# Kernel tuning notes

Hardware: AMD Instinct MI355X
Metric: run time of the kernel (lower is better)

## Reference

```python
import jax, jax.numpy as jnp
import numpy as np

N, T, I, H = 32, 2048, 256, 512


def setup_inputs() -> dict:
    key = jax.random.key(0)
    k1, k2, k3, k4, k5 = jax.random.split(key, 5)
    x = jax.random.normal(k1, (N, T, I), dtype=jnp.float32)
    initial = jax.random.normal(k2, (N, H), dtype=jnp.float32)
    # nn.Linear default init: U(-1/sqrt(fan_in), 1/sqrt(fan_in))
    s_ih = 1.0 / np.sqrt(I)
    s_hh = 1.0 / np.sqrt(H)
    W_ih = jax.random.uniform(k3, (H, I), jnp.float32, -s_ih, s_ih)
    b_ih = jax.random.uniform(k4, (H,), jnp.float32, -s_ih, s_ih)
    W_hh = jax.random.uniform(k5, (H, H), jnp.float32, -s_hh, s_hh)
    return {"x": x, "initial": initial, "W_ih": W_ih, "b_ih": b_ih, "W_hh": W_hh}


def reference(x, initial, W_ih, b_ih, W_hh):
    # Precompute input projections for all timesteps: [N, T, H]
    proj = jnp.einsum('nti,hi->nth', x, W_ih) + b_ih
    # h_0 = initial + W_ih x_0 + b
    h0 = initial + proj[:, 0]
    # h_t = W_hh h_{t-1} + W_ih x_{t-1} + b  (note: x index is t-1, faithful to source)
    xs = jnp.swapaxes(proj[:, :-1], 0, 1)  # time-major [T-1, N, H], entries t=0..T-2

    def step(h_prev, p):
        h_new = h_prev @ W_hh.T + p
        return h_new, h_new

    _, hs = jax.lax.scan(step, h0, xs)  # [T-1, N, H]
    hiddens = jnp.concatenate([h0[:, None], jnp.swapaxes(hs, 0, 1)], axis=1)  # [N, T, H]
    return (hiddens, hiddens)
```

## Files before the change

### kernel.cpp

```cpp
#include <hip/hip_runtime.h>

#define NB 32
#define TT 2048
#define II 256
#define HH 512
#define LCH 8
#define NCH 256

typedef short s8v __attribute__((ext_vector_type(8)));
typedef short s4v __attribute__((ext_vector_type(4)));
typedef __bf16 bf8v __attribute__((ext_vector_type(8)));
typedef float f4v __attribute__((ext_vector_type(4)));

#define DEVI static __device__ __forceinline__

DEVI float bf2f(short s){ union{unsigned u; float f;} c; c.u = ((unsigned)(unsigned short)s) << 16; return c.f; }
DEVI short f2bf(float f){ union{float f; unsigned u;} c; c.f = f; unsigned u = c.u; u += 0x7FFF + ((u >> 16) & 1); return (short)(u >> 16); }
DEVI f4v fzero(){ f4v z = {0.0f,0.0f,0.0f,0.0f}; return z; }

DEVI f4v mfma16(s8v a, s8v b, f4v c){
  union{ s8v s; bf8v b; } ua, ub; ua.s = a; ub.s = b;
  return __builtin_amdgcn_mfma_f32_16x16x32_bf16(ua.b, ub.b, c, 0, 0, 0);
}

DEVI s8v packbf(f4v lo, f4v hi){
  s8v o;
  o[0]=f2bf(lo[0]); o[1]=f2bf(lo[1]); o[2]=f2bf(lo[2]); o[3]=f2bf(lo[3]);
  o[4]=f2bf(hi[0]); o[5]=f2bf(hi[1]); o[6]=f2bf(hi[2]); o[7]=f2bf(hi[3]);
  return o;
}

DEVI s8v ldfrag_bf(const short* base, int row0, int ld, int k0, int lane){
  const short* p = base + (size_t)(row0 + (lane & 15)) * ld + k0 + ((lane >> 4) << 3);
  return *(const s8v*)p;
}
DEVI s8v ldfrag_f32(const float* base, int row0, int ld, int k0, int lane){
  const float* p = base + (size_t)(row0 + (lane & 15)) * ld + k0 + ((lane >> 4) << 3);
  f4v lo = *(const f4v*)p;
  f4v hi = *(const f4v*)(p + 4);
  return packbf(lo, hi);
}
DEVI s8v ldfragX(const float* x, int t, int n0, int k0, int lane){
  const float* p = x + ((size_t)(n0 + (lane & 15))*TT + t)*II + k0 + ((lane >> 4) << 3);
  f4v lo = *(const f4v*)p;
  f4v hi = *(const f4v*)(p + 4);
  return packbf(lo, hi);
}

DEVI int swzoff(int row, int col){ return (row << 9) + ((((col >> 3) ^ (row & 7)) << 3) | (col & 7)); }

#define RAWBAR() asm volatile("s_waitcnt lgkmcnt(0)\n\ts_barrier" ::: "memory")

__global__ __launch_bounds__(256) void k_init_p1(const float* __restrict__ W,
                                                 short* __restrict__ mats, short* __restrict__ matsT){
  __shared__ short tile[64][65];
  int bx = blockIdx.x, by = blockIdx.y;
  int t = threadIdx.x;
  for(int i = 0; i < 16; ++i){
    int idx = t + 256*i;
    int rr = idx >> 6, cc = idx & 63;
    short v = f2bf(W[(size_t)(64*by + rr)*HH + 64*bx + cc]);
    tile[rr][cc] = v;
    mats[(size_t)(64*by + rr)*HH + 64*bx + cc] = v;
  }
  __syncthreads();
  for(int i = 0; i < 16; ++i){
    int idx = t + 256*i;
    int rr = idx >> 6, cc = idx & 63;
    matsT[(size_t)(64*bx + rr)*HH + 64*by + cc] = tile[cc][rr];
  }
}

__global__ __launch_bounds__(256) void k_cvt(const float* __restrict__ src, short* __restrict__ dst, int n){
  for(int i = blockIdx.x*256 + threadIdx.x; i < n; i += gridDim.x*256) dst[i] = f2bf(src[i]);
}

struct ProdArgs {
  const short* A[8]; const short* Bt[8]; short* C[8]; short* Ct[8];
};
__global__ __launch_bounds__(256) void k_prod(ProdArgs args){
  int bz = blockIdx.z;
  const short* A  = args.A[bz];
  const short* Bt = args.Bt[bz];
  short* C  = args.C[bz];
  short* Ct = args.Ct[bz];
  int wave = threadIdx.x >> 6, lane = threadIdx.x & 63;
  int mrow0 = blockIdx.x*64 + (wave & 1)*32;
  int ncol0 = blockIdx.y*128 + (wave >> 1)*64;
  f4v acc[2][4];
  for(int mi=0;mi<2;mi++) for(int j=0;j<4;j++) acc[mi][j] = fzero();
  for(int k0 = 0; k0 < HH; k0 += 32){
    s8v a0 = ldfrag_bf(A, mrow0,      HH, k0, lane);
    s8v a1 = ldfrag_bf(A, mrow0 + 16, HH, k0, lane);
    #pragma unroll
    for(int j = 0; j < 4; ++j){
      s8v b = ldfrag_bf(Bt, ncol0 + (j<<4), HH, k0, lane);
      acc[0][j] = mfma16(a0, b, acc[0][j]);
      acc[1][j] = mfma16(a1, b, acc[1][j]);
    }
  }
  int q = lane >> 4, c0 = lane & 15;
  for(int mi=0;mi<2;mi++) for(int j=0;j<4;j++) for(int r=0;r<4;r++){
    int row = mrow0 + (mi<<4) + (q<<2) + r;
    int col = ncol0 + (j<<4) + c0;
    short v = f2bf(acc[mi][j][r]);
    C [(size_t)row*HH + col] = v;
    Ct[(size_t)col*HH + row] = v;
  }
}

__global__ __launch_bounds__(512) void k_projT(const float* __restrict__ x, const short* __restrict__ Wb,
                                               const float* __restrict__ bih, const float* __restrict__ initial,
                                               short* __restrict__ projF, float* __restrict__ Y00){
  int t = blockIdx.x;
  int tid = threadIdx.x, wave = tid >> 6, lane = tid & 63;
  int q = lane >> 4, c0 = lane & 15;
  int ncol0 = wave << 6;
  f4v acc[2][4];
  #pragma unroll
  for(int mi=0;mi<2;mi++)
  #pragma unroll
  for(int j=0;j<4;j++) acc[mi][j] = fzero();
  #pragma unroll
  for(int kc = 0; kc < 8; ++kc){
    int k0 = kc << 5;
    s8v a0 = ldfragX(x, t, 0,  k0, lane);
    s8v a1 = ldfragX(x, t, 16, k0, lane);
    #pragma unroll
    for(int j = 0; j < 4; ++j){
      s8v bb = ldfrag_bf(Wb, ncol0 + (j<<4), II, k0, lane);
      acc[0][j] = mfma16(a0, bb, acc[0][j]);
      acc[1][j] = mfma16(a1, bb, acc[1][j]);
    }
  }
  float bv[4];
  #pragma unroll
  for(int j=0;j<4;++j) bv[j] = bih[ncol0 + (j<<4) + c0];
  s8v pv[4];
  #pragma unroll
  for(int mi=0;mi<2;++mi)
  #pragma unroll
  for(int j=0;j<4;++j)
  #pragma unroll
  for(int r=0;r<4;++r){
    int idx = (mi<<4) | (j<<2) | r;
    float v = acc[mi][j][r] + bv[j];
    pv[idx>>3][idx&7] = f2bf(v);
    if(t == 0){
      int n = (mi<<4) + (q<<2) + r;
      int col = ncol0 + (j<<4) + c0;
      Y00[(size_t)n*HH + col] = v + initial[(size_t)n*HH + col];
    }
  }
  short* dst = projF + (((size_t)t << 9) + tid)*32;
  #pragma unroll
  for(int g = 0; g < 4; ++g) *(s8v*)(dst + (g<<3)) = pv[g];
}

template<int PHASE, int DUAL>
__global__ __launch_bounds__(512) void k_scan(const short* __restrict__ projF,
                                              const short* __restrict__ Wb,
                                              const float* __restrict__ Zin,
                                              float* __restrict__ Yout,
                                              float* __restrict__ Yout2){
  __shared__ __align__(16) short st[NB*HH];
  __shared__ __align__(16) float fstage[PHASE==1 ? NB*HH : 4];
  int c = blockIdx.x;
  int tid = threadIdx.x, wave = tid >> 6, lane = tid & 63;
  int q = lane >> 4, c0 = lane & 15;
  int ncol0 = wave << 6;
  if constexpr(PHASE == 0){
    for(int i = tid; i < NB*HH; i += 512) st[i] = 0;
  } else {
    const float* Z = Zin + (size_t)c*NB*HH;
    #pragma unroll
    for(int rr = 0; rr < 8; ++rr){
      int fi = tid + (rr << 9);
      int rn = fi >> 7, col = (fi & 127) << 2;
      f4v v = *(const f4v*)(Z + (size_t)rn*HH + col);
      s4v sv; sv[0]=f2bf(v[0]); sv[1]=f2bf(v[1]); sv[2]=f2bf(v[2]); sv[3]=f2bf(v[3]);
      *(s4v*)(st + swzoff(rn, col)) = sv;
      if(c == 0){
        *(f4v*)(Yout + ((size_t)rn*TT)*HH + col) = v;
        if(DUAL) *(f4v*)(Yout2 + ((size_t)rn*TT)*HH + col) = v;
      }
    }
  }
  RAWBAR();
  int tmax = min(LCH, TT - 1 - LCH*c);
  for(int tl = 1; tl <= tmax; ++tl){
    int t = LCH*c + tl;
    const short* pb = projF + (((size_t)(t-1) << 9) + tid)*32;
    s8v pp[4];
    pp[0] = *(const s8v*)(pb);
    pp[1] = *(const s8v*)(pb + 8);
    pp[2] = *(const s8v*)(pb + 16);
    pp[3] = *(const s8v*)(pb + 24);
    f4v acc[2][4];
    #pragma unroll
    for(int mi=0;mi<2;mi++)
    #pragma unroll
    for(int j=0;j<4;j++) acc[mi][j] = fzero();
    #pragma unroll
    for(int kc = 0; kc < 16; ++kc){
      int k0 = kc << 5;
      int colb = k0 + (q << 3);
      s8v a0 = *(const s8v*)(st + swzoff(c0,      colb));
      s8v a1 = *(const s8v*)(st + swzoff(c0 + 16, colb));
      #pragma unroll
      for(int j = 0; j < 4; ++j){
        s8v bb = ldfrag_bf(Wb, ncol0 + (j<<4), HH, k0, lane);
        acc[0][j] = mfma16(a0, bb, acc[0][j]);
        acc[1][j] = mfma16(a1, bb, acc[1][j]);
      }
    }
    RAWBAR();
    #pragma unroll
    for(int mi=0;mi<2;++mi)
    #pragma unroll
    for(int j=0;j<4;++j)
    #pragma unroll
    for(int r=0;r<4;++r){
      int idx = (mi<<4) | (j<<2) | r;
      int rown = (mi<<4) + (q<<2) + r;
      int col  = ncol0 + (j<<4) + c0;
      float v = acc[mi][j][r] + bf2f(pp[idx>>3][idx&7]);
      st[swzoff(rown, col)] = f2bf(v);
      if constexpr(PHASE == 0){
        if(tl == LCH && c + 1 < NCH)
          Yout[((size_t)(c+1)*NB + rown)*HH + col] = v;
      } else {
        fstage[rown*HH + col] = v;
      }
    }
    if constexpr(PHASE == 1){
      RAWBAR();
      #pragma unroll
      for(int rr = 0; rr < 8; ++rr){
        int fi = tid + (rr << 9);
        int rn = fi >> 7, col = (fi & 127) << 2;
        f4v v = *(const f4v*)(fstage + (size_t)rn*HH + col);
        *(f4v*)(Yout + ((size_t)rn*TT + t)*HH + col) = v;
        if(DUAL) *(f4v*)(Yout2 + ((size_t)rn*TT + t)*HH + col) = v;
      }
    } else {
      RAWBAR();
    }
  }
}

__global__ __launch_bounds__(512) void k_ks(const float* __restrict__ Yin, float* __restrict__ Yout,
                                            const short* __restrict__ As, int s){
  __shared__ __align__(16) float fstage[NB*HH];
  int i = blockIdx.x;
  int tid = threadIdx.x;
  if(i < s){
    const float* src = Yin + (size_t)i*NB*HH;
    float* dst = Yout + (size_t)i*NB*HH;
    for(int fi = tid; fi < NB*HH/4; fi += 512)
      *(f4v*)(dst + ((size_t)fi << 2)) = *(const f4v*)(src + ((size_t)fi << 2));
    return;
  }
  int wave = tid >> 6, lane = tid & 63;
  int q = lane >> 4, c0 = lane & 15;
  int ncol0 = wave << 6;
  const float* Xp = Yin + (size_t)(i - s)*NB*HH;
  const float* Xc = Yin + (size_t)i*NB*HH;
  float* Out = Yout + (size_t)i*NB*HH;
  f4v acc[2][4];
  #pragma unroll
  for(int mi=0;mi<2;mi++)
  #pragma unroll
  for(int j=0;j<4;j++) acc[mi][j] = fzero();
  #pragma unroll
  for(int kc = 0; kc < 16; ++kc){
    int k0 = kc << 5;
    s8v a0 = ldfrag_f32(Xp, 0,  HH, k0, lane);
    s8v a1 = ldfrag_f32(Xp, 16, HH, k0, lane);
    #pragma unroll
    for(int j = 0; j < 4; ++j){
      s8v bb = ldfrag_bf(As, ncol0 + (j<<4), HH, k0, lane);
      acc[0][j] = mfma16(a0, bb, acc[0][j]);
      acc[1][j] = mfma16(a1, bb, acc[1][j]);
    }
  }
  #pragma unroll
  for(int mi=0;mi<2;++mi)
  #pragma unroll
  for(int j=0;j<4;++j)
  #pragma unroll
  for(int r=0;r<4;++r){
    int rown = (mi<<4) + (q<<2) + r;
    int col  = ncol0 + (j<<4) + c0;
    fstage[(size_t)rown*HH + col] = acc[mi][j][r];
  }
  RAWBAR();
  #pragma unroll
  for(int rr = 0; rr < 8; ++rr){
    int fi = tid + (rr << 9);
    int rn = fi >> 7, col = (fi & 127) << 2;
    f4v v = *(const f4v*)(fstage + (size_t)rn*HH + col);
    f4v xc = *(const f4v*)(Xc + (size_t)rn*HH + col);
    v = v + xc;
    *(f4v*)(Out + (size_t)rn*HH + col) = v;
  }
}

__global__ __launch_bounds__(256) void k_dup(const float* __restrict__ a, float* __restrict__ b, int n4){
  for(int i = blockIdx.x*256 + threadIdx.x; i < n4; i += gridDim.x*256)
    ((f4v*)b)[i] = ((const f4v*)a)[i];
}

extern "C" void kernel_launch(void* const* d_in, const int* in_sizes, int n_in,
                              void* d_out, int out_size, void* d_ws, size_t ws_size,
                              hipStream_t stream) {
  const float* x       = (const float*)d_in[0];
  const float* initial = (const float*)d_in[1];
  const float* Wih     = (const float*)d_in[2];
  const float* bih     = (const float*)d_in[3];
  const float* Whh     = (const float*)d_in[4];
  float* out1 = (float*)d_out;
  float* out2 = out1 + (size_t)NB*TT*HH;

  const size_t MSZ = (size_t)HH*HH;
  short* mats  = (short*)d_ws;
  short* matsT = mats + 11*MSZ;
  short* Wihb  = matsT + 11*MSZ;
  float* Y0 = (float*)(Wihb + (size_t)HH*II);
  float* Y1 = out1;
  short* projw = (short*)(Y0 + (size_t)NCH*NB*HH);
  size_t need = (size_t)((char*)(projw + (size_t)NB*TT*HH) - (char*)d_ws);
  bool dual = ws_size >= need;
  short* projF = dual ? projw : (short*)out2;

  auto M = [&](int i){ return mats  + (size_t)i*MSZ; };
  auto T = [&](int i){ return matsT + (size_t)i*MSZ; };

  k_init_p1<<<dim3(8,8), 256, 0, stream>>>(Whh, M(0), T(0));
  k_cvt<<<dim3(64), 256, 0, stream>>>(Wih, Wihb, HH*II);

  ProdArgs pa;
  for(int i = 0; i < 10; ++i){
    pa.A[0] = M(i); pa.Bt[0] = T(i); pa.C[0] = M(i+1); pa.Ct[0] = T(i+1);
    k_prod<<<dim3(8,4,1), 256, 0, stream>>>(pa);
  }

  k_projT<<<dim3(TT), 512, 0, stream>>>(x, Wihb, bih, initial, projF, Y0);
  k_scan<0,0><<<dim3(NCH), 512, 0, stream>>>(projF, M(0), nullptr, Y0, nullptr);

  float* Ya = Y0; float* Yb = Y1;
  for(int l = 0; l < 8; ++l){
    k_ks<<<dim3(NCH), 512, 0, stream>>>(Ya, Yb, M(3 + l), 1 << l);
    float* tsw = Ya; Ya = Yb; Yb = tsw;
  }

  if(dual){
    k_scan<1,1><<<dim3(NCH), 512, 0, stream>>>(projF, M(0), Y0, out1, out2);
  } else {
    k_scan<1,0><<<dim3(NCH), 512, 0, stream>>>(projF, M(0), Y0, out1, out1);
    k_dup<<<dim3(2048), 256, 0, stream>>>(out1, out2, NB*TT*HH/4);
  }
}
```

Measured before the change: 1.296 ms.

## Use nontemporal loads/stores for streaming data and drop LDS output staging in scan

Replaces ordinary global loads and stores of streamed activations, projections and outputs with nontemporal builtins across the projection, scan and Kogge-Stone kernels, to reduce cache pollution. In the phase-1 scan it also removes the fp32 LDS staging buffer and extra barrier, writing each output element straight to global memory with scalar nontemporal stores. This cuts LDS use and a barrier per timestep, but the direct scalar stores are less coalesced than the old vectorized staged writes.

Measured after the change: 1.443 ms. +11.4%, slower.

```diff
diff --git a/kernel.cpp b/kernel.cpp
--- a/kernel.cpp
+++ b/kernel.cpp
@@ -18,6 +18,12 @@
 DEVI short f2bf(float f){ union{float f; unsigned u;} c; c.f = f; unsigned u = c.u; u += 0x7FFF + ((u >> 16) & 1); return (short)(u >> 16); }
 DEVI f4v fzero(){ f4v z = {0.0f,0.0f,0.0f,0.0f}; return z; }
 
+DEVI f4v ntl_f4(const float* p){ return __builtin_nontemporal_load((const f4v*)p); }
+DEVI s8v ntl_s8(const short* p){ return __builtin_nontemporal_load((const s8v*)p); }
+DEVI void nts_f4(float* p, f4v v){ __builtin_nontemporal_store(v, (f4v*)p); }
+DEVI void nts_f(float* p, float v){ __builtin_nontemporal_store(v, p); }
+DEVI void nts_s8(short* p, s8v v){ __builtin_nontemporal_store(v, (s8v*)p); }
+
 DEVI f4v mfma16(s8v a, s8v b, f4v c){
   union{ s8v s; bf8v b; } ua, ub; ua.s = a; ub.s = b;
   return __builtin_amdgcn_mfma_f32_16x16x32_bf16(ua.b, ub.b, c, 0, 0, 0);
@@ -34,17 +40,13 @@
   const short* p = base + (size_t)(row0 + (lane & 15)) * ld + k0 + ((lane >> 4) << 3);
   return *(const s8v*)p;
 }
-DEVI s8v ldfrag_f32(const float* base, int row0, int ld, int k0, int lane){
+DEVI s8v ldfrag_f32_nt(const float* base, int row0, int ld, int k0, int lane){
   const float* p = base + (size_t)(row0 + (lane & 15)) * ld + k0 + ((lane >> 4) << 3);
-  f4v lo = *(const f4v*)p;
-  f4v hi = *(const f4v*)(p + 4);
-  return packbf(lo, hi);
+  return packbf(ntl_f4(p), ntl_f4(p + 4));
 }
 DEVI s8v ldfragX(const float* x, int t, int n0, int k0, int lane){
   const float* p = x + ((size_t)(n0 + (lane & 15))*TT + t)*II + k0 + ((lane >> 4) << 3);
-  f4v lo = *(const f4v*)p;
-  f4v hi = *(const f4v*)(p + 4);
-  return packbf(lo, hi);
+  return packbf(ntl_f4(p), ntl_f4(p + 4));
 }
 
 DEVI int swzoff(int row, int col){ return (row << 9) + ((((col >> 3) ^ (row & 7)) << 3) | (col & 7)); }
@@ -154,7 +156,7 @@
   }
   short* dst = projF + (((size_t)t << 9) + tid)*32;
   #pragma unroll
-  for(int g = 0; g < 4; ++g) *(s8v*)(dst + (g<<3)) = pv[g];
+  for(int g = 0; g < 4; ++g) nts_s8(dst + (g<<3), pv[g]);
 }
 
 template<int PHASE, int DUAL>
@@ -164,7 +166,6 @@
                                               float* __restrict__ Yout,
                                               float* __restrict__ Yout2){
   __shared__ __align__(16) short st[NB*HH];
-  __shared__ __align__(16) float fstage[PHASE==1 ? NB*HH : 4];
   int c = blockIdx.x;
   int tid = threadIdx.x, wave = tid >> 6, lane = tid & 63;
   int q = lane >> 4, c0 = lane & 15;
@@ -177,12 +178,12 @@
     for(int rr = 0; rr < 8; ++rr){
       int fi = tid + (rr << 9);
       int rn = fi >> 7, col = (fi & 127) << 2;
-      f4v v = *(const f4v*)(Z + (size_t)rn*HH + col);
+      f4v v = ntl_f4(Z + (size_t)rn*HH + col);
       s4v sv; sv[0]=f2bf(v[0]); sv[1]=f2bf(v[1]); sv[2]=f2bf(v[2]); sv[3]=f2bf(v[3]);
       *(s4v*)(st + swzoff(rn, col)) = sv;
       if(c == 0){
-        *(f4v*)(Yout + ((size_t)rn*TT)*HH + col) = v;
-        if(DUAL) *(f4v*)(Yout2 + ((size_t)rn*TT)*HH + col) = v;
+        nts_f4(Yout + ((size_t)rn*TT)*HH + col, v);
+        if(DUAL) nts_f4(Yout2 + ((size_t)rn*TT)*HH + col, v);
       }
     }
   }
@@ -192,10 +193,10 @@
     int t = LCH*c + tl;
     const short* pb = projF + (((size_t)(t-1) << 9) + tid)*32;
     s8v pp[4];
-    pp[0] = *(const s8v*)(pb);
-    pp[1] = *(const s8v*)(pb + 8);
-    pp[2] = *(const s8v*)(pb + 16);
-    pp[3] = *(const s8v*)(pb + 24);
+    pp[0] = ntl_s8(pb);
+    pp[1] = ntl_s8(pb + 8);
+    pp[2] = ntl_s8(pb + 16);
+    pp[3] = ntl_s8(pb + 24);
     f4v acc[2][4];
     #pragma unroll
     for(int mi=0;mi<2;mi++)
@@ -228,24 +229,13 @@
       st[swzoff(rown, col)] = f2bf(v);
       if constexpr(PHASE == 0){
         if(tl == LCH && c + 1 < NCH)
-          Yout[((size_t)(c+1)*NB + rown)*HH + col] = v;
+          nts_f(Yout + (((size_t)(c+1)*NB + rown)*HH + col), v);
       } else {
-        fstage[rown*HH + col] = v;
+        nts_f(Yout + (((size_t)rown*TT + t)*HH + col), v);
+        if(DUAL) nts_f(Yout2 + (((size_t)rown*TT + t)*HH + col), v);
       }
     }
-    if constexpr(PHASE == 1){
-      RAWBAR();
-      #pragma unroll
-      for(int rr = 0; rr < 8; ++rr){
-        int fi = tid + (rr << 9);
-        int rn = fi >> 7, col = (fi & 127) << 2;
-        f4v v = *(const f4v*)(fstage + (size_t)rn*HH + col);
-        *(f4v*)(Yout + ((size_t)rn*TT + t)*HH + col) = v;
-        if(DUAL) *(f4v*)(Yout2 + ((size_t)rn*TT + t)*HH + col) = v;
-      }
-    } else {
-      RAWBAR();
-    }
+    RAWBAR();
   }
 }
 
@@ -258,7 +248,7 @@
     const float* src = Yin + (size_t)i*NB*HH;
     float* dst = Yout + (size_t)i*NB*HH;
     for(int fi = tid; fi < NB*HH/4; fi += 512)
-      *(f4v*)(dst + ((size_t)fi << 2)) = *(const f4v*)(src + ((size_t)fi << 2));
+      nts_f4(dst + ((size_t)fi << 2), ntl_f4(src + ((size_t)fi << 2)));
     return;
   }
   int wave = tid >> 6, lane = tid & 63;
@@ -275,8 +265,8 @@
   #pragma unroll
   for(int kc = 0; kc < 16; ++kc){
     int k0 = kc << 5;
-    s8v a0 = ldfrag_f32(Xp, 0,  HH, k0, lane);
-    s8v a1 = ldfrag_f32(Xp, 16, HH, k0, lane);
+    s8v a0 = ldfrag_f32_nt(Xp, 0,  HH, k0, lane);
+    s8v a1 = ldfrag_f32_nt(Xp, 16, HH, k0, lane);
     #pragma unroll
     for(int j = 0; j < 4; ++j){
       s8v bb = ldfrag_bf(As, ncol0 + (j<<4), HH, k0, lane);
@@ -284,14 +274,15 @@
       acc[1][j] = mfma16(a1, bb, acc[1][j]);
     }
   }
+  int q2 = lane >> 4, c02 = lane & 15;
   #pragma unroll
   for(int mi=0;mi<2;++mi)
   #pragma unroll
   for(int j=0;j<4;++j)
   #pragma unroll
   for(int r=0;r<4;++r){
-    int rown = (mi<<4) + (q<<2) + r;
-    int col  = ncol0 + (j<<4) + c0;
+    int rown = (mi<<4) + (q2<<2) + r;
+    int col  = ncol0 + (j<<4) + c02;
     fstage[(size_t)rown*HH + col] = acc[mi][j][r];
   }
   RAWBAR();
@@ -300,9 +291,9 @@
     int fi = tid + (rr << 9);
     int rn = fi >> 7, col = (fi & 127) << 2;
     f4v v = *(const f4v*)(fstage + (size_t)rn*HH + col);
-    f4v xc = *(const f4v*)(Xc + (size_t)rn*HH + col);
+    f4v xc = ntl_f4(Xc + (size_t)rn*HH + col);
     v = v + xc;
-    *(f4v*)(Out + (size_t)rn*HH + col) = v;
+    nts_f4(Out + (size_t)rn*HH + col, v);
   }
 }
 
```

## Halve scan chunk length, stage W_hh tiles in LDS, add Kogge-Stone level

Applied to the files above, without the earlier changes.

Chunk length drops from 8 to 4 steps and the chunk count doubles to 512, so the sequential scan kernels do less serial work per block. The Kogge-Stone combine gains a ninth level and uses matrix powers starting one index lower. The scan kernels now stream W_hh k-slices into LDS with global_load_lds and XOR swizzling instead of loading B fragments straight from global memory. Phase-1 writes results directly to global memory rather than through an fp32 LDS staging buffer. The costs are an extra KS pass over twice as many chunk states, more barriers per step, and a second workspace Y buffer; the final KS output must land in Yw, which holds because nine levels is an odd number of buffer swaps.

New measurement: 1.695 ms. 30.8% more time.

```diff
diff --git a/kernel.cpp b/kernel.cpp
--- a/kernel.cpp
+++ b/kernel.cpp
@@ -4,8 +4,9 @@
 #define TT 2048
 #define II 256
 #define HH 512
-#define LCH 8
-#define NCH 256
+#define LCH 4
+#define NCH 512
+#define KSL 9
 
 typedef short s8v __attribute__((ext_vector_type(8)));
 typedef short s4v __attribute__((ext_vector_type(4)));
@@ -50,6 +51,27 @@
 DEVI int swzoff(int row, int col){ return (row << 9) + ((((col >> 3) ^ (row & 7)) << 3) | (col & 7)); }
 
 #define RAWBAR() asm volatile("s_waitcnt lgkmcnt(0)\n\ts_barrier" ::: "memory")
+
+DEVI void gload16(const void* g, void* l){
+  __builtin_amdgcn_global_load_lds((const __attribute__((address_space(1))) void*)g,
+                                   (__attribute__((address_space(3))) void*)l, 16, 0, 0);
+}
+
+DEVI int xw(int col){ return (col & 3) ^ ((col >> 2) & 3); }
+
+DEVI void stageC(const short* Wb, int k0, short* btile, int wave, int lane){
+  #pragma unroll
+  for(int r = 0; r < 4; ++r){
+    int sb = (r << 9) + (wave << 6);
+    int s  = sb + lane;
+    int col = s >> 2, g = s & 3;
+    int gsrc = g ^ xw(col);
+    gload16(Wb + (size_t)col*HH + k0 + (gsrc << 3), btile + ((size_t)sb << 3));
+  }
+}
+DEVI s8v ldC(const short* btile, int col, int q){
+  return *(const s8v*)(btile + (col << 5) + ((q ^ xw(col)) << 3));
+}
 
 __global__ __launch_bounds__(256) void k_init_p1(const float* __restrict__ W,
                                                  short* __restrict__ mats, short* __restrict__ matsT){
@@ -158,13 +180,13 @@
 }
 
 template<int PHASE, int DUAL>
-__global__ __launch_bounds__(512) void k_scan(const short* __restrict__ projF,
-                                              const short* __restrict__ Wb,
-                                              const float* __restrict__ Zin,
-                                              float* __restrict__ Yout,
-                                              float* __restrict__ Yout2){
+__global__ __launch_bounds__(512, 4) void k_scan(const short* __restrict__ projF,
+                                                 const short* __restrict__ Wb,
+                                                 const float* __restrict__ Zin,
+                                                 float* __restrict__ Yout,
+                                                 float* __restrict__ Yout2){
   __shared__ __align__(16) short st[NB*HH];
-  __shared__ __align__(16) float fstage[PHASE==1 ? NB*HH : 4];
+  __shared__ __align__(16) short btile[HH*32];
   int c = blockIdx.x;
   int tid = threadIdx.x, wave = tid >> 6, lane = tid & 63;
   int q = lane >> 4, c0 = lane & 15;
@@ -190,31 +212,32 @@
   int tmax = min(LCH, TT - 1 - LCH*c);
   for(int tl = 1; tl <= tmax; ++tl){
     int t = LCH*c + tl;
+    f4v acc[2][4];
+    #pragma unroll
+    for(int mi=0;mi<2;mi++)
+    #pragma unroll
+    for(int j=0;j<4;j++) acc[mi][j] = fzero();
+    #pragma unroll
+    for(int kc = 0; kc < 16; ++kc){
+      stageC(Wb, kc << 5, btile, wave, lane);
+      __syncthreads();
+      int colb = (kc << 5) + (q << 3);
+      s8v a0 = *(const s8v*)(st + swzoff(c0,      colb));
+      s8v a1 = *(const s8v*)(st + swzoff(c0 + 16, colb));
+      #pragma unroll
+      for(int j = 0; j < 4; ++j){
+        s8v bb = ldC(btile, ncol0 + (j<<4) + c0, q);
+        acc[0][j] = mfma16(a0, bb, acc[0][j]);
+        acc[1][j] = mfma16(a1, bb, acc[1][j]);
+      }
+      RAWBAR();
+    }
     const short* pb = projF + (((size_t)(t-1) << 9) + tid)*32;
     s8v pp[4];
     pp[0] = *(const s8v*)(pb);
     pp[1] = *(const s8v*)(pb + 8);
     pp[2] = *(const s8v*)(pb + 16);
     pp[3] = *(const s8v*)(pb + 24);
-    f4v acc[2][4];
-    #pragma unroll
-    for(int mi=0;mi<2;mi++)
-    #pragma unroll
-    for(int j=0;j<4;j++) acc[mi][j] = fzero();
-    #pragma unroll
-    for(int kc = 0; kc < 16; ++kc){
-      int k0 = kc << 5;
-      int colb = k0 + (q << 3);
-      s8v a0 = *(const s8v*)(st + swzoff(c0,      colb));
-      s8v a1 = *(const s8v*)(st + swzoff(c0 + 16, colb));
-      #pragma unroll
-      for(int j = 0; j < 4; ++j){
-        s8v bb = ldfrag_bf(Wb, ncol0 + (j<<4), HH, k0, lane);
-        acc[0][j] = mfma16(a0, bb, acc[0][j]);
-        acc[1][j] = mfma16(a1, bb, acc[1][j]);
-      }
-    }
-    RAWBAR();
     #pragma unroll
     for(int mi=0;mi<2;++mi)
     #pragma unroll
@@ -230,27 +253,16 @@
         if(tl == LCH && c + 1 < NCH)
           Yout[((size_t)(c+1)*NB + rown)*HH + col] = v;
       } else {
-        fstage[rown*HH + col] = v;
+        Yout[((size_t)rown*TT + t)*HH + col] = v;
+        if(DUAL) Yout2[((size_t)rown*TT + t)*HH + col] = v;
       }
     }
-    if constexpr(PHASE == 1){
-      RAWBAR();
-      #pragma unroll
-      for(int rr = 0; rr < 8; ++rr){
-        int fi = tid + (rr << 9);
-        int rn = fi >> 7, col = (fi & 127) << 2;
-        f4v v = *(const f4v*)(fstage + (size_t)rn*HH + col);
-        *(f4v*)(Yout + ((size_t)rn*TT + t)*HH + col) = v;
-        if(DUAL) *(f4v*)(Yout2 + ((size_t)rn*TT + t)*HH + col) = v;
-      }
-    } else {
-      RAWBAR();
-    }
-  }
-}
-
-__global__ __launch_bounds__(512) void k_ks(const float* __restrict__ Yin, float* __restrict__ Yout,
-                                            const short* __restrict__ As, int s){
+    RAWBAR();
+  }
+}
+
+__global__ __launch_bounds__(512, 4) void k_ks(const float* __restrict__ Yin, float* __restrict__ Yout,
+                                               const short* __restrict__ As, int s){
   __shared__ __align__(16) float fstage[NB*HH];
   int i = blockIdx.x;
   int tid = threadIdx.x;
@@ -323,15 +335,17 @@
   float* out2 = out1 + (size_t)NB*TT*HH;
 
   const size_t MSZ = (size_t)HH*HH;
+  const size_t YSZ = (size_t)NCH*NB*HH;
   short* mats  = (short*)d_ws;
   short* matsT = mats + 11*MSZ;
   short* Wihb  = matsT + 11*MSZ;
   float* Y0 = (float*)(Wihb + (size_t)HH*II);
-  float* Y1 = out1;
-  short* projw = (short*)(Y0 + (size_t)NCH*NB*HH);
+  float* Ywq = Y0 + YSZ;
+  short* projw = (short*)(Ywq + YSZ);
   size_t need = (size_t)((char*)(projw + (size_t)NB*TT*HH) - (char*)d_ws);
   bool dual = ws_size >= need;
   short* projF = dual ? projw : (short*)out2;
+  float* Yw    = dual ? Ywq   : (float*)((short*)out2 + (size_t)NB*TT*HH);
 
   auto M = [&](int i){ return mats  + (size_t)i*MSZ; };
   auto T = [&](int i){ return matsT + (size_t)i*MSZ; };
@@ -348,16 +362,16 @@
   k_projT<<<dim3(TT), 512, 0, stream>>>(x, Wihb, bih, initial, projF, Y0);
   k_scan<0,0><<<dim3(NCH), 512, 0, stream>>>(projF, M(0), nullptr, Y0, nullptr);
 
-  float* Ya = Y0; float* Yb = Y1;
-  for(int l = 0; l < 8; ++l){
-    k_ks<<<dim3(NCH), 512, 0, stream>>>(Ya, Yb, M(3 + l), 1 << l);
+  float* Ya = Y0; float* Yb = Yw;
+  for(int l = 0; l < KSL; ++l){
+    k_ks<<<dim3(NCH), 512, 0, stream>>>(Ya, Yb, M(2 + l), 1 << l);
     float* tsw = Ya; Ya = Yb; Yb = tsw;
   }
 
   if(dual){
-    k_scan<1,1><<<dim3(NCH), 512, 0, stream>>>(projF, M(0), Y0, out1, out2);
+    k_scan<1,1><<<dim3(NCH), 512, 0, stream>>>(projF, M(0), Yw, out1, out2);
   } else {
-    k_scan<1,0><<<dim3(NCH), 512, 0, stream>>>(projF, M(0), Y0, out1, out1);
+    k_scan<1,0><<<dim3(NCH), 512, 0, stream>>>(projF, M(0), Yw, out1, out1);
     k_dup<<<dim3(2048), 256, 0, stream>>>(out1, out2, NB*TT*HH/4);
   }
 }
```
